# Optimization experiments

Hardware: AMD Instinct MI355X
Metric: run time of the kernel (lower is better)

The kernel has to match this reference:

```python
import jax, jax.numpy as jnp
import numpy as np

N_HEADS = 32
N_KV_HEADS = 8
THETA = 10000.0


def _rope_tables(head_dim, seq_len):
    # freqs: [head_dim//2]
    freqs = 1.0 / (THETA ** (jnp.arange(0, head_dim, 2, dtype=jnp.float32) / head_dim))
    ang = jnp.arange(seq_len, dtype=jnp.float32)[:, None] * freqs[None, :]  # [T, hd/2]
    return jnp.cos(ang), jnp.sin(ang)


def _apply_rope(x, cos, sin):
    # x: [B, T, H, hd]; cos/sin: [T, hd/2] -> broadcast [1, T, 1, hd/2]
    x_even = x[..., 0::2]
    x_odd = x[..., 1::2]
    c = cos[None, :, None, :]
    s = sin[None, :, None, :]
    out_even = x_even * c - x_odd * s
    out_odd = x_even * s + x_odd * c
    # interleave back to [..., hd]
    out = jnp.stack([out_even, out_odd], axis=-1)
    return out.reshape(x.shape)


def setup_inputs() -> dict:
    key = jax.random.key(0)
    ks = jax.random.split(key, 5)
    B, T, C = 2, 2048, 2048
    kv_dim = (C // N_HEADS) * N_KV_HEADS  # 512
    sc = 1.0 / np.sqrt(C)
    return {
        "x": jax.random.normal(ks[0], (B, T, C), dtype=jnp.float32),
        "wq": jax.random.normal(ks[1], (C, C), dtype=jnp.float32) * sc,
        "wk": jax.random.normal(ks[2], (C, kv_dim), dtype=jnp.float32) * sc,
        "wv": jax.random.normal(ks[3], (C, kv_dim), dtype=jnp.float32) * sc,
        "wo": jax.random.normal(ks[4], (C, C), dtype=jnp.float32) * sc,
    }


def reference(x, wq, wk, wv, wo):
    B, T, C = x.shape
    hd = C // N_HEADS
    rep = N_HEADS // N_KV_HEADS

    q = (x @ wq).reshape(B, T, N_HEADS, hd)
    k = (x @ wk).reshape(B, T, N_KV_HEADS, hd)
    v = (x @ wv).reshape(B, T, N_KV_HEADS, hd)

    cos, sin = _rope_tables(hd, T)
    q = _apply_rope(q, cos, sin)
    k = _apply_rope(k, cos, sin)

    q = q.transpose(0, 2, 1, 3)  # [B, H, T, hd]
    k = k.transpose(0, 2, 1, 3)  # [B, KV, T, hd]
    v = v.transpose(0, 2, 1, 3)

    # GQA: repeat_interleave kv heads to match q heads
    k = jnp.repeat(k, rep, axis=1)
    v = jnp.repeat(v, rep, axis=1)

    scores = jnp.einsum("bhtd,bhsd->bhts", q, k) / jnp.sqrt(jnp.float32(hd))
    weights = jax.nn.softmax(scores, axis=-1)  # no causal mask, as in source
    out = jnp.einsum("bhts,bhsd->bhtd", weights, v)
    out = out.transpose(0, 2, 1, 3).reshape(B, T, C)
    return out @ wo
```

## Files before the change

kernel.cpp:

```cpp
#include <hip/hip_runtime.h>
#include <hip/hip_bf16.h>


typedef unsigned short u16;
typedef short bf16x8 __attribute__((ext_vector_type(8)));
typedef float f32x4 __attribute__((ext_vector_type(4)));
typedef unsigned uint32x4 __attribute__((ext_vector_type(4)));

#define LOG2E 1.4426950408889634f
#define NFREQ (-13.287712379549449f / 32.f)

#if __has_builtin(__builtin_amdgcn_exp2f)
#define EXP2F(x) __builtin_amdgcn_exp2f(x)
#else
#define EXP2F(x) exp2f(x)
#endif

__device__ __forceinline__ float bf2f(u16 u) {
    union { unsigned v; float f; } x; x.v = ((unsigned)u) << 16; return x.f;
}
__device__ __forceinline__ u16 f2bf(float f) {
    unsigned u = __float_as_uint(f);
    u += 0x7fffu + ((u >> 16) & 1u);
    return (u16)(u >> 16);
}
__device__ __forceinline__ unsigned cvt_pk_bf16(float lo, float hi) {
    unsigned r;
    asm("v_cvt_pk_bf16_f32 %0, %1, %2" : "=v"(r) : "v"(lo), "v"(hi));
    return r;
}

__device__ __forceinline__ void async_copy16(const void* g, void* l) {
    __builtin_amdgcn_global_load_lds((const __attribute__((address_space(1))) void*)g,
                                     (__attribute__((address_space(3))) void*)l, 16, 0, 0);
}

__global__ void prep_kernel(const float* __restrict__ x,
                            const float* __restrict__ wq, const float* __restrict__ wk,
                            const float* __restrict__ wv, const float* __restrict__ wo,
                            u16* __restrict__ xbf, u16* __restrict__ wqkvT,
                            u16* __restrict__ woT, float2* __restrict__ rtab) {
    const int bz = blockIdx.z;
    if (bz < 4) {
        const int K = 2048;
        const float* W; u16* Wt; int N;
        switch (bz) {
            case 0:  W = wq; Wt = wqkvT;                        N = 2048; break;
            case 1:  W = wk; Wt = wqkvT + (size_t)2048 * 2048;  N = 512;  break;
            case 2:  W = wv; Wt = wqkvT + (size_t)2560 * 2048;  N = 512;  break;
            default: W = wo; Wt = woT;                          N = 2048; break;
        }
        if ((int)blockIdx.x * 32 >= N) return;
        __shared__ float tile[32][33];
        int xx = blockIdx.x * 32 + threadIdx.x;
        int y0 = blockIdx.y * 32 + threadIdx.y;
        #pragma unroll
        for (int r = 0; r < 32; r += 8)
            tile[threadIdx.y + r][threadIdx.x] = W[(size_t)(y0 + r) * N + xx];
        __syncthreads();
        int xo = blockIdx.y * 32 + threadIdx.x;
        int yo0 = blockIdx.x * 32 + threadIdx.y;
        #pragma unroll
        for (int r = 0; r < 32; r += 8)
            Wt[(size_t)(yo0 + r) * K + xo] = f2bf(tile[threadIdx.x][threadIdx.y + r]);
    } else if (bz == 4) {
        int bid = blockIdx.y * gridDim.x + blockIdx.x;
        int tid = threadIdx.y * 32 + threadIdx.x;
        const size_t n4 = (size_t)4096 * 2048 / 4;
        for (size_t i = (size_t)bid * 256 + tid; i < n4; i += (size_t)4096 * 256) {
            float4 v = ((const float4*)x)[i];
            ushort4 o;
            o.x = f2bf(v.x); o.y = f2bf(v.y); o.z = f2bf(v.z); o.w = f2bf(v.w);
            ((ushort4*)xbf)[i] = o;
        }
    } else {
        int bid = blockIdx.y * gridDim.x + blockIdx.x;
        int idx = bid * 256 + threadIdx.y * 32 + threadIdx.x;
        if (idx < 2048 * 32) {
            int t = idx >> 5, i = idx & 31;
            float freq = exp2f((float)i * NFREQ);
            float s, c;
            sincosf((float)t * freq, &s, &c);
            rtab[idx] = make_float2(c, s);
        }
    }
}

__global__ void transpose_perm_kernel(const u16* __restrict__ in, u16* __restrict__ out,
                                      int R, int C) {
    __shared__ u16 tile[32][33];
    int xx = blockIdx.x * 32 + threadIdx.x;
    int y0 = blockIdx.y * 32;
    #pragma unroll
    for (int r = threadIdx.y; r < 32; r += 8)
        tile[r][threadIdx.x] = in[(size_t)(y0 + r) * C + xx];
    __syncthreads();
    int s = y0 + threadIdx.x;
    int c = s & 127;
    int sp = (s & ~127) | (c & 96) | ((c & 12) << 1) | ((c & 16) >> 2) | (c & 3);
    int yo = blockIdx.x * 32;
    #pragma unroll
    for (int r = threadIdx.y; r < 32; r += 8)
        out[(size_t)(yo + r) * R + sp] = tile[threadIdx.x][r];
}

__global__ __launch_bounds__(256) void gemm_qkv_kernel(const u16* __restrict__ A,
                                                       const u16* __restrict__ Bt,
                                                       u16* __restrict__ qout,
                                                       u16* __restrict__ kout,
                                                       u16* __restrict__ vout,
                                                       const float2* __restrict__ rope_tab,
                                                       int K) {
    __shared__ __align__(16) u16 As[128 * 64];
    __shared__ __align__(16) u16 Bs[128 * 64];
    const int tid = threadIdx.x;
    const int m0 = blockIdx.y * 128;
    const int n0 = blockIdx.x * 128;
    const int w = tid >> 6, lane = tid & 63;
    const int quad = lane >> 4, ln = lane & 15;
    const int wr = (w >> 1) * 64, wc = (w & 1) * 64;

    f32x4 acc[4][4];
    #pragma unroll
    for (int i = 0; i < 4; i++)
        #pragma unroll
        for (int j = 0; j < 4; j++) acc[i][j] = (f32x4){0.f, 0.f, 0.f, 0.f};

    for (int kt = 0; kt < K; kt += 64) {
        #pragma unroll
        for (int p = 0; p < 4; p++) {
            int chunk = p * 256 + tid;
            int r = chunk >> 3, cl = chunk & 7;
            int cg = cl ^ (r & 7);
            async_copy16(&A[(size_t)(m0 + r) * K + kt + cg * 8], &As[chunk * 8]);
            async_copy16(&Bt[(size_t)(n0 + r) * K + kt + cg * 8], &Bs[chunk * 8]);
        }
        __syncthreads();
        #pragma unroll
        for (int kk = 0; kk < 2; kk++) {
            bf16x8 a[4], b[4];
            #pragma unroll
            for (int i = 0; i < 4; i++) {
                int r = wr + i * 16 + ln;
                int cl = (kk * 4 + quad) ^ (ln & 7);
                a[i] = *(const bf16x8*)(&As[r * 64 + cl * 8]);
            }
            #pragma unroll
            for (int j = 0; j < 4; j++) {
                int r = wc + j * 16 + ln;
                int cl = (kk * 4 + quad) ^ (ln & 7);
                b[j] = *(const bf16x8*)(&Bs[r * 64 + cl * 8]);
            }
            #pragma unroll
            for (int i = 0; i < 4; i++)
                #pragma unroll
                for (int j = 0; j < 4; j++)
                    acc[i][j] = __builtin_amdgcn_mfma_f32_16x16x32_bf16(a[i], b[j], acc[i][j], 0, 0, 0);
        }
        __syncthreads();
    }

    int nb = n0 + wc;
    u16* dst; int ldc, coff; bool isv = false; float scale = 1.f;
    if (nb < 2048)      { dst = qout; ldc = 2048; coff = 0;    scale = 0.125f * LOG2E; }
    else if (nb < 2560) { dst = kout; ldc = 512;  coff = 2048; }
    else                { dst = vout; ldc = 512;  coff = 2560; isv = true; }

    if (isv) {
        #pragma unroll
        for (int i = 0; i < 4; i++)
            #pragma unroll
            for (int r = 0; r < 4; r++) {
                int row = m0 + wr + i * 16 + quad * 4 + r;
                #pragma unroll
                for (int j = 0; j < 4; j++)
                    dst[(size_t)row * ldc + nb + j * 16 + ln - coff] = f2bf(acc[i][j][r]);
            }
    } else {
        float fsin = (ln & 1) ? 1.f : -1.f;
        int fidx[4];
        #pragma unroll
        for (int j = 0; j < 4; j++)
            fidx[j] = ((nb + j * 16 + ln) & 63) >> 1;
        #pragma unroll
        for (int i = 0; i < 4; i++)
            #pragma unroll
            for (int r = 0; r < 4; r++) {
                int row = m0 + wr + i * 16 + quad * 4 + r;
                const float2* trow = rope_tab + (size_t)(row & 2047) * 32;
                #pragma unroll
                for (int j = 0; j < 4; j++) {
                    float v = acc[i][j][r];
                    float p = __shfl_xor(v, 1, 64);
                    float2 cs = trow[fidx[j]];
                    float rr = (v * cs.x + fsin * p * cs.y) * scale;
                    dst[(size_t)row * ldc + nb + j * 16 + ln - coff] = f2bf(rr);
                }
            }
    }
}

__global__ __launch_bounds__(256) void gemm_bt_kernel(const u16* __restrict__ A,
                                                      const u16* __restrict__ Bt,
                                                      float* __restrict__ C,
                                                      int M, int N, int K) {
    __shared__ __align__(16) u16 As[128 * 64];
    __shared__ __align__(16) u16 Bs[128 * 64];
    const int tid = threadIdx.x;
    const int m0 = blockIdx.y * 128;
    const int n0 = blockIdx.x * 128;
    const int w = tid >> 6, lane = tid & 63;
    const int quad = lane >> 4, ln = lane & 15;
    const int wr = (w >> 1) * 64, wc = (w & 1) * 64;

    f32x4 acc[4][4];
    #pragma unroll
    for (int i = 0; i < 4; i++)
        #pragma unroll
        for (int j = 0; j < 4; j++) acc[i][j] = (f32x4){0.f, 0.f, 0.f, 0.f};

    for (int kt = 0; kt < K; kt += 64) {
        #pragma unroll
        for (int p = 0; p < 4; p++) {
            int chunk = p * 256 + tid;
            int r = chunk >> 3, cl = chunk & 7;
            int cg = cl ^ (r & 7);
            async_copy16(&A[(size_t)(m0 + r) * K + kt + cg * 8], &As[chunk * 8]);
            async_copy16(&Bt[(size_t)(n0 + r) * K + kt + cg * 8], &Bs[chunk * 8]);
        }
        __syncthreads();
        #pragma unroll
        for (int kk = 0; kk < 2; kk++) {
            bf16x8 a[4], b[4];
            #pragma unroll
            for (int i = 0; i < 4; i++) {
                int r = wr + i * 16 + ln;
                int cl = (kk * 4 + quad) ^ (ln & 7);
                a[i] = *(const bf16x8*)(&As[r * 64 + cl * 8]);
            }
            #pragma unroll
            for (int j = 0; j < 4; j++) {
                int r = wc + j * 16 + ln;
                int cl = (kk * 4 + quad) ^ (ln & 7);
                b[j] = *(const bf16x8*)(&Bs[r * 64 + cl * 8]);
            }
            #pragma unroll
            for (int i = 0; i < 4; i++)
                #pragma unroll
                for (int j = 0; j < 4; j++)
                    acc[i][j] = __builtin_amdgcn_mfma_f32_16x16x32_bf16(a[i], b[j], acc[i][j], 0, 0, 0);
        }
        __syncthreads();
    }
    #pragma unroll
    for (int i = 0; i < 4; i++)
        #pragma unroll
        for (int r = 0; r < 4; r++) {
            int row = m0 + wr + i * 16 + quad * 4 + r;
            #pragma unroll
            for (int j = 0; j < 4; j++)
                C[(size_t)row * N + n0 + wc + j * 16 + ln] = acc[i][j][r];
        }
}

__global__ __launch_bounds__(256) void attn_kernel(const u16* __restrict__ qb,
                                                   const u16* __restrict__ kb,
                                                   const u16* __restrict__ vtb,
                                                   u16* __restrict__ ob) {
    const int T = 2048;
    const int CQ = 2048, CKV = 512;
    __shared__ __align__(16) u16 Ks[2][128 * 64];
    __shared__ __align__(16) u16 Vt[2][64 * 128];

    const int tid = threadIdx.x;
    const int bh = blockIdx.y;
    const int b = bh >> 5, h = bh & 31, kvh = h >> 2;
    const int t0 = blockIdx.x * 128;
    const u16* qbase = qb + ((size_t)(b * T + t0) * CQ + h * 64);
    const u16* kbase = kb + ((size_t)(b * T) * CKV + kvh * 64);
    const u16* vtbase = vtb + ((size_t)(kvh * 64)) * 4096 + b * 2048;

    const int w = tid >> 6, lane = tid & 63, quad = lane >> 4, ln = lane & 15;

    bf16x8 ones;
    #pragma unroll
    for (int e = 0; e < 8; e++) ones[e] = (short)0x3F80;

    const u16* kp[4]; const u16* vp[4];
    int chunks[4];
    #pragma unroll
    for (int p = 0; p < 4; p++) {
        int chunk = p * 256 + tid;
        chunks[p] = chunk;
        int r = chunk >> 3, cl = chunk & 7;
        int cg = cl ^ (r & 7);
        kp[p] = kbase + (size_t)r * CKV + cg * 8;
        int d = chunk >> 4, cl2 = chunk & 15;
        int cg2 = cl2 ^ (d & 7);
        vp[p] = vtbase + (size_t)d * 4096 + cg2 * 8;
    }

    bf16x8 qf[2][2];
    #pragma unroll
    for (int i = 0; i < 2; i++)
        #pragma unroll
        for (int kk = 0; kk < 2; kk++)
            qf[i][kk] = *(const bf16x8*)(&qbase[(size_t)(w * 32 + i * 16 + ln) * CQ + kk * 32 + quad * 8]);

    f32x4 o_acc[2][4];
    f32x4 l_acc[2];
    #pragma unroll
    for (int i = 0; i < 2; i++) {
        l_acc[i] = (f32x4){0.f, 0.f, 0.f, 0.f};
        #pragma unroll
        for (int j = 0; j < 4; j++) o_acc[i][j] = (f32x4){0.f, 0.f, 0.f, 0.f};
    }
    const f32x4 zero4 = (f32x4){0.f, 0.f, 0.f, 0.f};

    #pragma unroll
    for (int p = 0; p < 4; p++) {
        async_copy16(kp[p], &Ks[0][chunks[p] * 8]);
        async_copy16(vp[p], &Vt[0][chunks[p] * 8]);
        kp[p] += 128 * CKV;
        vp[p] += 128;
    }
    __syncthreads();

    int cur = 0;
    for (int st = 0; st < T; st += 128) {
        if (st + 128 < T) {
            #pragma unroll
            for (int p = 0; p < 4; p++) {
                async_copy16(kp[p], &Ks[cur ^ 1][chunks[p] * 8]);
                async_copy16(vp[p], &Vt[cur ^ 1][chunks[p] * 8]);
                kp[p] += 128 * CKV;
                vp[p] += 128;
            }
        }
        const u16* KsC = Ks[cur];
        const u16* VtC = Vt[cur];

        f32x4 s_acc[8][2];
        {
            bf16x8 kf[8];
            #pragma unroll
            for (int j = 0; j < 8; j++) {
                int r = j * 16 + ln;
                int cl = quad ^ (ln & 7);
                kf[j] = *(const bf16x8*)(&KsC[r * 64 + cl * 8]);
            }
            __builtin_amdgcn_s_setprio(1);
            #pragma unroll
            for (int j = 0; j < 8; j++)
                #pragma unroll
                for (int i = 0; i < 2; i++)
                    s_acc[j][i] = __builtin_amdgcn_mfma_f32_16x16x32_bf16(kf[j], qf[i][0], zero4, 0, 0, 0);
            __builtin_amdgcn_s_setprio(0);
        }
        {
            bf16x8 kf[8];
            #pragma unroll
            for (int j = 0; j < 8; j++) {
                int r = j * 16 + ln;
                int cl = (4 + quad) ^ (ln & 7);
                kf[j] = *(const bf16x8*)(&KsC[r * 64 + cl * 8]);
            }
            __builtin_amdgcn_s_setprio(1);
            #pragma unroll
            for (int j = 0; j < 8; j++)
                #pragma unroll
                for (int i = 0; i < 2; i++)
                    s_acc[j][i] = __builtin_amdgcn_mfma_f32_16x16x32_bf16(kf[j], qf[i][1], s_acc[j][i], 0, 0, 0);
            __builtin_amdgcn_s_setprio(0);
        }

        bf16x8 pa[2][4];
        #pragma unroll
        for (int i = 0; i < 2; i++)
            #pragma unroll
            for (int c = 0; c < 4; c++) {
                unsigned w0 = cvt_pk_bf16(EXP2F(s_acc[2 * c][i][0]),     EXP2F(s_acc[2 * c][i][1]));
                unsigned w1 = cvt_pk_bf16(EXP2F(s_acc[2 * c][i][2]),     EXP2F(s_acc[2 * c][i][3]));
                unsigned w2 = cvt_pk_bf16(EXP2F(s_acc[2 * c + 1][i][0]), EXP2F(s_acc[2 * c + 1][i][1]));
                unsigned w3 = cvt_pk_bf16(EXP2F(s_acc[2 * c + 1][i][2]), EXP2F(s_acc[2 * c + 1][i][3]));
                union { uint32x4 u; bf16x8 b; } pu;
                pu.u = (uint32x4){w0, w1, w2, w3};
                pa[i][c] = pu.b;
            }

        #pragma unroll
        for (int c = 0; c < 4; c++) {
            bf16x8 vb[4];
            #pragma unroll
            for (int jd = 0; jd < 4; jd++) {
                int d = jd * 16 + ln;
                int cg = c * 4 + quad;
                int cl = (cg & 8) | ((cg ^ (d & 7)) & 7);
                vb[jd] = *(const bf16x8*)(&VtC[d * 128 + cl * 8]);
            }
            __builtin_amdgcn_s_setprio(1);
            #pragma unroll
            for (int i = 0; i < 2; i++) {
                l_acc[i] = __builtin_amdgcn_mfma_f32_16x16x32_bf16(pa[i][c], ones, l_acc[i], 0, 0, 0);
                #pragma unroll
                for (int jd = 0; jd < 4; jd++)
                    o_acc[i][jd] = __builtin_amdgcn_mfma_f32_16x16x32_bf16(pa[i][c], vb[jd], o_acc[i][jd], 0, 0, 0);
            }
            __builtin_amdgcn_s_setprio(0);
        }

        __syncthreads();
        cur ^= 1;
    }

    #pragma unroll
    for (int i = 0; i < 2; i++)
        #pragma unroll
        for (int rr = 0; rr < 4; rr++) {
            float linv = 1.f / l_acc[i][rr];
            int row = w * 32 + i * 16 + quad * 4 + rr;
            #pragma unroll
            for (int jd = 0; jd < 4; jd++) {
                int col = jd * 16 + ln;
                ob[(size_t)(b * T + t0 + row) * CQ + h * 64 + col] = f2bf(o_acc[i][jd][rr] * linv);
            }
        }
}

#define WS_X_BF   ((size_t)0)
#define WS_WQKVT  ((size_t)16777216)
#define WS_WOT    ((size_t)29360128)
#define WS_QBF    ((size_t)37748736)
#define WS_KBF    ((size_t)54525952)
#define WS_VBF    ((size_t)58720256)
#define WS_ABF    ((size_t)62914560)

extern "C" void kernel_launch(void* const* d_in, const int* in_sizes, int n_in,
                              void* d_out, int out_size, void* d_ws, size_t ws_size,
                              hipStream_t stream) {
    const float* x  = (const float*)d_in[0];
    const float* wq = (const float*)d_in[1];
    const float* wk = (const float*)d_in[2];
    const float* wv = (const float*)d_in[3];
    const float* wo = (const float*)d_in[4];
    char* ws = (char*)d_ws;
    u16* xbf   = (u16*)(ws + WS_X_BF);
    u16* wqkvT = (u16*)(ws + WS_WQKVT);
    u16* woT   = (u16*)(ws + WS_WOT);
    u16* qbf   = (u16*)(ws + WS_QBF);
    u16* kbf   = (u16*)(ws + WS_KBF);
    u16* vbf   = (u16*)(ws + WS_VBF);
    u16* vtbf  = (u16*)(ws + WS_X_BF);
    u16* abf   = (u16*)(ws + WS_ABF);
    float2* rtab = (float2*)(ws + WS_ABF);
    float* out = (float*)d_out;

    prep_kernel<<<dim3(64, 64, 6), dim3(32, 8), 0, stream>>>(x, wq, wk, wv, wo,
                                                             xbf, wqkvT, woT, rtab);

    gemm_qkv_kernel<<<dim3(24, 32), 256, 0, stream>>>(xbf, wqkvT, qbf, kbf, vbf, rtab, 2048);

    transpose_perm_kernel<<<dim3(16, 128), dim3(32, 8), 0, stream>>>(vbf, vtbf, 4096, 512);

    attn_kernel<<<dim3(16, 64), 256, 0, stream>>>(qbf, kbf, vtbf, abf);

    gemm_bt_kernel<<<dim3(16, 32), 256, 0, stream>>>(abf, woT, out, 4096, 2048, 2048);
}
```

Before: 313.7 us.

## Fuse V transpose into QKV GEMM epilogue and enlarge attention blocks

The QKV GEMM epilogue now writes V directly in the transposed, permuted layout the attention kernel expects, with vectorized 4-element stores, so the separate transpose kernel and its extra pass over V are gone. The attention kernel moves to 512 threads per block covering 256 query rows, which halves how often each K/V tile is loaded across blocks. The cost is fewer attention blocks (512), which may lower occupancy or leave compute units less evenly loaded.

Result: no change. 310.5 us (-1.0%).

```diff
diff --git a/kernel.cpp b/kernel.cpp
--- a/kernel.cpp
+++ b/kernel.cpp
@@ -86,29 +86,11 @@
     }
 }
 
-__global__ void transpose_perm_kernel(const u16* __restrict__ in, u16* __restrict__ out,
-                                      int R, int C) {
-    __shared__ u16 tile[32][33];
-    int xx = blockIdx.x * 32 + threadIdx.x;
-    int y0 = blockIdx.y * 32;
-    #pragma unroll
-    for (int r = threadIdx.y; r < 32; r += 8)
-        tile[r][threadIdx.x] = in[(size_t)(y0 + r) * C + xx];
-    __syncthreads();
-    int s = y0 + threadIdx.x;
-    int c = s & 127;
-    int sp = (s & ~127) | (c & 96) | ((c & 12) << 1) | ((c & 16) >> 2) | (c & 3);
-    int yo = blockIdx.x * 32;
-    #pragma unroll
-    for (int r = threadIdx.y; r < 32; r += 8)
-        out[(size_t)(yo + r) * R + sp] = tile[threadIdx.x][r];
-}
-
 __global__ __launch_bounds__(256) void gemm_qkv_kernel(const u16* __restrict__ A,
                                                        const u16* __restrict__ Bt,
                                                        u16* __restrict__ qout,
                                                        u16* __restrict__ kout,
-                                                       u16* __restrict__ vout,
+                                                       u16* __restrict__ vtout,
                                                        const float2* __restrict__ rope_tab,
                                                        int K) {
     __shared__ __align__(16) u16 As[128 * 64];
@@ -161,43 +143,46 @@
     }
 
     int nb = n0 + wc;
-    u16* dst; int ldc, coff; bool isv = false; float scale = 1.f;
-    if (nb < 2048)      { dst = qout; ldc = 2048; coff = 0;    scale = 0.125f * LOG2E; }
-    else if (nb < 2560) { dst = kout; ldc = 512;  coff = 2048; }
-    else                { dst = vout; ldc = 512;  coff = 2560; isv = true; }
-
-    if (isv) {
-        #pragma unroll
-        for (int i = 0; i < 4; i++)
-            #pragma unroll
-            for (int r = 0; r < 4; r++) {
-                int row = m0 + wr + i * 16 + quad * 4 + r;
-                #pragma unroll
-                for (int j = 0; j < 4; j++)
-                    dst[(size_t)row * ldc + nb + j * 16 + ln - coff] = f2bf(acc[i][j][r]);
-            }
-    } else {
-        float fsin = (ln & 1) ? 1.f : -1.f;
-        int fidx[4];
-        #pragma unroll
-        for (int j = 0; j < 4; j++)
-            fidx[j] = ((nb + j * 16 + ln) & 63) >> 1;
-        #pragma unroll
-        for (int i = 0; i < 4; i++)
-            #pragma unroll
-            for (int r = 0; r < 4; r++) {
-                int row = m0 + wr + i * 16 + quad * 4 + r;
-                const float2* trow = rope_tab + (size_t)(row & 2047) * 32;
-                #pragma unroll
-                for (int j = 0; j < 4; j++) {
-                    float v = acc[i][j][r];
-                    float p = __shfl_xor(v, 1, 64);
-                    float2 cs = trow[fidx[j]];
-                    float rr = (v * cs.x + fsin * p * cs.y) * scale;
-                    dst[(size_t)row * ldc + nb + j * 16 + ln - coff] = f2bf(rr);
-                }
-            }
-    }
+    if (nb >= 2560) {
+        #pragma unroll
+        for (int i = 0; i < 4; i++) {
+            int cb = wr + i * 16 + quad * 4;
+            int sp0 = (cb & 96) | ((cb & 12) << 1) | ((cb & 16) >> 2);
+            #pragma unroll
+            for (int j = 0; j < 4; j++) {
+                int d = nb + j * 16 + ln - 2560;
+                ushort4 o;
+                o.x = f2bf(acc[i][j][0]); o.y = f2bf(acc[i][j][1]);
+                o.z = f2bf(acc[i][j][2]); o.w = f2bf(acc[i][j][3]);
+                *(ushort4*)(&vtout[(size_t)d * 4096 + m0 + sp0]) = o;
+            }
+        }
+        return;
+    }
+    u16* dst; int ldc, coff; float scale = 1.f;
+    if (nb < 2048) { dst = qout; ldc = 2048; coff = 0;    scale = 0.125f * LOG2E; }
+    else           { dst = kout; ldc = 512;  coff = 2048; }
+
+    float fsin = (ln & 1) ? 1.f : -1.f;
+    int fidx[4];
+    #pragma unroll
+    for (int j = 0; j < 4; j++)
+        fidx[j] = ((nb + j * 16 + ln) & 63) >> 1;
+    #pragma unroll
+    for (int i = 0; i < 4; i++)
+        #pragma unroll
+        for (int r = 0; r < 4; r++) {
+            int row = m0 + wr + i * 16 + quad * 4 + r;
+            const float2* trow = rope_tab + (size_t)(row & 2047) * 32;
+            #pragma unroll
+            for (int j = 0; j < 4; j++) {
+                float v = acc[i][j][r];
+                float p = __shfl_xor(v, 1, 64);
+                float2 cs = trow[fidx[j]];
+                float rr = (v * cs.x + fsin * p * cs.y) * scale;
+                dst[(size_t)row * ldc + nb + j * 16 + ln - coff] = f2bf(rr);
+            }
+        }
 }
 
 __global__ __launch_bounds__(256) void gemm_bt_kernel(const u16* __restrict__ A,
@@ -263,7 +248,7 @@
         }
 }
 
-__global__ __launch_bounds__(256) void attn_kernel(const u16* __restrict__ qb,
+__global__ __launch_bounds__(512) void attn_kernel(const u16* __restrict__ qb,
                                                    const u16* __restrict__ kb,
                                                    const u16* __restrict__ vtb,
                                                    u16* __restrict__ ob) {
@@ -275,7 +260,7 @@
     const int tid = threadIdx.x;
     const int bh = blockIdx.y;
     const int b = bh >> 5, h = bh & 31, kvh = h >> 2;
-    const int t0 = blockIdx.x * 128;
+    const int t0 = blockIdx.x * 256;
     const u16* qbase = qb + ((size_t)(b * T + t0) * CQ + h * 64);
     const u16* kbase = kb + ((size_t)(b * T) * CKV + kvh * 64);
     const u16* vtbase = vtb + ((size_t)(kvh * 64)) * 4096 + b * 2048;
@@ -286,11 +271,11 @@
     #pragma unroll
     for (int e = 0; e < 8; e++) ones[e] = (short)0x3F80;
 
-    const u16* kp[4]; const u16* vp[4];
-    int chunks[4];
-    #pragma unroll
-    for (int p = 0; p < 4; p++) {
-        int chunk = p * 256 + tid;
+    const u16* kp[2]; const u16* vp[2];
+    int chunks[2];
+    #pragma unroll
+    for (int p = 0; p < 2; p++) {
+        int chunk = p * 512 + tid;
         chunks[p] = chunk;
         int r = chunk >> 3, cl = chunk & 7;
         int cg = cl ^ (r & 7);
@@ -318,7 +303,7 @@
     const f32x4 zero4 = (f32x4){0.f, 0.f, 0.f, 0.f};
 
     #pragma unroll
-    for (int p = 0; p < 4; p++) {
+    for (int p = 0; p < 2; p++) {
         async_copy16(kp[p], &Ks[0][chunks[p] * 8]);
         async_copy16(vp[p], &Vt[0][chunks[p] * 8]);
         kp[p] += 128 * CKV;
@@ -330,7 +315,7 @@
     for (int st = 0; st < T; st += 128) {
         if (st + 128 < T) {
             #pragma unroll
-            for (int p = 0; p < 4; p++) {
+            for (int p = 0; p < 2; p++) {
                 async_copy16(kp[p], &Ks[cur ^ 1][chunks[p] * 8]);
                 async_copy16(vp[p], &Vt[cur ^ 1][chunks[p] * 8]);
                 kp[p] += 128 * CKV;
@@ -432,7 +417,7 @@
 #define WS_WOT    ((size_t)29360128)
 #define WS_QBF    ((size_t)37748736)
 #define WS_KBF    ((size_t)54525952)
-#define WS_VBF    ((size_t)58720256)
+#define WS_VTBF   ((size_t)58720256)
 #define WS_ABF    ((size_t)62914560)
 
 extern "C" void kernel_launch(void* const* d_in, const int* in_sizes, int n_in,
@@ -449,8 +434,7 @@
     u16* woT   = (u16*)(ws + WS_WOT);
     u16* qbf   = (u16*)(ws + WS_QBF);
     u16* kbf   = (u16*)(ws + WS_KBF);
-    u16* vbf   = (u16*)(ws + WS_VBF);
-    u16* vtbf  = (u16*)(ws + WS_X_BF);
+    u16* vtbf  = (u16*)(ws + WS_VTBF);
     u16* abf   = (u16*)(ws + WS_ABF);
     float2* rtab = (float2*)(ws + WS_ABF);
     float* out = (float*)d_out;
@@ -458,11 +442,9 @@
     prep_kernel<<<dim3(64, 64, 6), dim3(32, 8), 0, stream>>>(x, wq, wk, wv, wo,
                                                              xbf, wqkvT, woT, rtab);
 
-    gemm_qkv_kernel<<<dim3(24, 32), 256, 0, stream>>>(xbf, wqkvT, qbf, kbf, vbf, rtab, 2048);
-
-    transpose_perm_kernel<<<dim3(16, 128), dim3(32, 8), 0, stream>>>(vbf, vtbf, 4096, 512);
-
-    attn_kernel<<<dim3(16, 64), 256, 0, stream>>>(qbf, kbf, vtbf, abf);
+    gemm_qkv_kernel<<<dim3(24, 32), 256, 0, stream>>>(xbf, wqkvT, qbf, kbf, vtbf, rtab, 2048);
+
+    attn_kernel<<<dim3(8, 64), 512, 0, stream>>>(qbf, kbf, vtbf, abf);
 
     gemm_bt_kernel<<<dim3(16, 32), 256, 0, stream>>>(abf, woT, out, 4096, 2048, 2048);
 }
```
